# Kernel tuning notes

Hardware: AMD Instinct MI355X
Metric: run time of the kernel (lower is better)

Reference implementation:

```python
import jax, jax.numpy as jnp
import numpy as np


def setup_inputs() -> dict:
    key = jax.random.key(0)
    k1, k2 = jax.random.split(key)
    B, Lq, Ls, D = 16, 2048, 2048, 512
    query = jax.random.normal(k1, (B, Lq, D), dtype=jnp.float32)
    support = jax.random.normal(k2, (B, Ls, D), dtype=jnp.float32)
    return {"query": query, "support": support}


def reference(query, support):
    # attn: [B, Lq, Ls] = softmax(query @ support^T, axis=-1)
    logits = jnp.einsum("bqd,bsd->bqs", query, support)
    attn = jax.nn.softmax(logits, axis=-1)
    # attended support: [B, Lq, D]
    attended = jnp.einsum("bqs,bsd->bqd", attn, support)
    # score: [B, Lq] = sum over D of query * attended
    score = jnp.sum(query * attended, axis=-1)
    return score
```

## Files before the change

kernel.cpp:

```cpp
#include <hip/hip_runtime.h>
#include <hip/hip_bf16.h>

#define B_  16
#define LQ  2048
#define LS  2048
#define DD  512
#define BQ  128
#define BS  256
#define BK  64
#define NSB (LS / BS)
#define NKC (DD / BK)
#define NSPLIT 2

typedef short bf16x8 __attribute__((ext_vector_type(8)));
typedef float f32x4  __attribute__((ext_vector_type(4)));

__device__ __forceinline__ void load_lds16(const void* g, void* l) {
  __builtin_amdgcn_global_load_lds((const __attribute__((address_space(1))) void*)g,
                                   (__attribute__((address_space(3))) void*)l,
                                   16, 0, 0);
}

__device__ __forceinline__ unsigned short f2bf(float f) {
  union { float f; unsigned int u; } v; v.f = f;
  unsigned int r = v.u + 0x7fffu + ((v.u >> 16) & 1u);
  return (unsigned short)(r >> 16);
}

__global__ __launch_bounds__(256) void cvt_kernel(const float* __restrict__ Q,
                                                  const float* __restrict__ S,
                                                  unsigned short* __restrict__ Qw,
                                                  unsigned short* __restrict__ Sw,
                                                  int nblk) {
  int blk = blockIdx.x;
  const float* src; unsigned short* dst;
  if (blk < nblk) { src = Q; dst = Qw; } else { src = S; dst = Sw; blk -= nblk; }
  int i = blk * 256 + threadIdx.x;
  float4 f = ((const float4*)src)[i];
  ushort4 u;
  u.x = f2bf(f.x); u.y = f2bf(f.y); u.z = f2bf(f.z); u.w = f2bf(f.w);
  ((ushort4*)dst)[i] = u;
}

__global__ __launch_bounds__(1024, 4) void attn_kernel(const unsigned short* __restrict__ Qw,
                                                       const unsigned short* __restrict__ Sw,
                                                       float* __restrict__ out,
                                                       float* __restrict__ pm,
                                                       float* __restrict__ pse,
                                                       float* __restrict__ psel,
                                                       int nsplit) {
  __shared__ __align__(16) unsigned short sQ[2][BQ * BK];
  __shared__ __align__(16) unsigned short sS[2][BS * BK];

  const int qb   = blockIdx.x;
  const int b    = blockIdx.y;
  const int spl  = blockIdx.z;
  const int tid  = threadIdx.x;
  const int w    = tid >> 6;
  const int lane = tid & 63;
  const int h    = w & 3;
  const int g    = w >> 2;
  const int col  = lane & 15;
  const int quad = lane >> 4;
  const int c7   = col & 7;

  const int q0 = qb * BQ;
  const unsigned short* Qb = Qw + (size_t)b * LQ * DD;
  const unsigned short* Sb = Sw + (size_t)b * LS * DD;

  float mst[2] = { -INFINITY, -INFINITY };
  float se[2]  = { 0.f, 0.f };
  float sel[2] = { 0.f, 0.f };

  f32x4 acc[4][2];

  const int rr = lane >> 3;
  const int cc = ((lane & 7) ^ rr) * 8;

  const int sbp = NSB / nsplit;
  const int sbs = spl * sbp;
  const int T   = sbp * NKC;

  auto issue = [&](int t, int buf) {
    const int sb = sbs + (t >> 3);
    const int kc = t & 7;
    const int s0 = sb * BS;
    const int kb = kc * BK + cc;
    load_lds16(Qb + (size_t)(q0 + w * 8 + rr) * DD + kb,        &sQ[buf][(w * 8) * BK]);
    load_lds16(Sb + (size_t)(s0 + w * 8 + rr) * DD + kb,        &sS[buf][(w * 8) * BK]);
    load_lds16(Sb + (size_t)(s0 + 128 + w * 8 + rr) * DD + kb,  &sS[buf][(128 + w * 8) * BK]);
  };

  issue(0, 0);

  for (int t = 0; t < T; ++t) {
    const int buf = t & 1;
    __syncthreads();
    if (t + 1 < T) issue(t + 1, buf ^ 1);

    if ((t & 7) == 0) {
#pragma unroll
      for (int st = 0; st < 4; ++st)
#pragma unroll
        for (int qt = 0; qt < 2; ++qt)
          acc[st][qt] = (f32x4){0.f, 0.f, 0.f, 0.f};
    }

#pragma unroll
    for (int kk = 0; kk < 2; ++kk) {
      const int koff = ((kk * 4 + quad) ^ c7) * 8;
      bf16x8 aq[2], asv[4];
#pragma unroll
      for (int qt = 0; qt < 2; ++qt)
        aq[qt] = *(const bf16x8*)&sQ[buf][(g * 32 + qt * 16 + col) * BK + koff];
#pragma unroll
      for (int st = 0; st < 4; ++st)
        asv[st] = *(const bf16x8*)&sS[buf][(h * 64 + st * 16 + col) * BK + koff];
#pragma unroll
      for (int st = 0; st < 4; ++st)
#pragma unroll
        for (int qt = 0; qt < 2; ++qt)
          acc[st][qt] = __builtin_amdgcn_mfma_f32_16x16x32_bf16(asv[st], aq[qt], acc[st][qt], 0, 0, 0);
    }

    if ((t & 7) == 7) {
#pragma unroll
      for (int qt = 0; qt < 2; ++qt) {
        float lmax = mst[qt];
#pragma unroll
        for (int st = 0; st < 4; ++st)
#pragma unroll
          for (int r = 0; r < 4; ++r)
            lmax = fmaxf(lmax, acc[st][qt][r]);
        lmax = fmaxf(lmax, __shfl_xor(lmax, 16, 64));
        lmax = fmaxf(lmax, __shfl_xor(lmax, 32, 64));
        float alpha = __expf(mst[qt] - lmax);
        float pe = 0.f, pel = 0.f;
#pragma unroll
        for (int st = 0; st < 4; ++st)
#pragma unroll
          for (int r = 0; r < 4; ++r) {
            float l = acc[st][qt][r];
            float e = __expf(l - lmax);
            pe += e;
            pel = fmaf(e, l, pel);
          }
        pe  += __shfl_xor(pe, 16, 64);  pe  += __shfl_xor(pe, 32, 64);
        pel += __shfl_xor(pel, 16, 64); pel += __shfl_xor(pel, 32, 64);
        se[qt]  = fmaf(se[qt],  alpha, pe);
        sel[qt] = fmaf(sel[qt], alpha, pel);
        mst[qt] = lmax;
      }
    }
  }

  __syncthreads();
  float* red = (float*)&sQ[0][0];
  if (quad == 0) {
#pragma unroll
    for (int qt = 0; qt < 2; ++qt) {
      int idx = ((g * 4 + h) * 2 + qt) * 16 + col;
      red[idx]        = mst[qt];
      red[512 + idx]  = se[qt];
      red[1024 + idx] = sel[qt];
    }
  }
  __syncthreads();
  if (h == 0 && quad == 0) {
#pragma unroll
    for (int qt = 0; qt < 2; ++qt) {
      float M = -INFINITY;
#pragma unroll
      for (int hh = 0; hh < 4; ++hh)
        M = fmaxf(M, red[((g * 4 + hh) * 2 + qt) * 16 + col]);
      float SE = 0.f, SEL = 0.f;
#pragma unroll
      for (int hh = 0; hh < 4; ++hh) {
        int idx = ((g * 4 + hh) * 2 + qt) * 16 + col;
        float a = __expf(red[idx] - M);
        SE  = fmaf(red[512 + idx],  a, SE);
        SEL = fmaf(red[1024 + idx], a, SEL);
      }
      size_t qi = (size_t)b * LQ + q0 + g * 32 + qt * 16 + col;
      if (nsplit == 1) {
        out[qi] = SEL / SE;
      } else {
        pm[qi * NSPLIT + spl]   = M;
        pse[qi * NSPLIT + spl]  = SE;
        psel[qi * NSPLIT + spl] = SEL;
      }
    }
  }
}

__global__ __launch_bounds__(256) void combine_kernel(const float* __restrict__ pm,
                                                      const float* __restrict__ pse,
                                                      const float* __restrict__ psel,
                                                      float* __restrict__ out) {
  int i = blockIdx.x * blockDim.x + threadIdx.x;
  if (i >= B_ * LQ) return;
  float M = -INFINITY;
#pragma unroll
  for (int s = 0; s < NSPLIT; ++s) M = fmaxf(M, pm[i * NSPLIT + s]);
  float SE = 0.f, SEL = 0.f;
#pragma unroll
  for (int s = 0; s < NSPLIT; ++s) {
    float a = __expf(pm[i * NSPLIT + s] - M);
    SE  = fmaf(pse[i * NSPLIT + s],  a, SE);
    SEL = fmaf(psel[i * NSPLIT + s], a, SEL);
  }
  out[i] = SEL / SE;
}

__global__ __launch_bounds__(256) void fallback_kernel(const float* __restrict__ Q,
                                                       const float* __restrict__ S,
                                                       float* __restrict__ out) {
  __shared__ float qv[DD];
  __shared__ float red[256];
  const int b = blockIdx.y, qi = blockIdx.x, tid = threadIdx.x;
  const float* qrow = Q + ((size_t)b * LQ + qi) * DD;
  for (int d = tid; d < DD; d += 256) qv[d] = qrow[d];
  __syncthreads();
  const float* Sb = S + (size_t)b * LS * DD;
  float m = -INFINITY, se = 0.f, sel = 0.f;
  for (int s = tid; s < LS; s += 256) {
    const float* srow = Sb + (size_t)s * DD;
    float dot = 0.f;
    for (int d = 0; d < DD; ++d) dot = fmaf(qv[d], srow[d], dot);
    float mn = fmaxf(m, dot);
    float a = __expf(m - mn);
    float e = __expf(dot - mn);
    se  = se * a + e;
    sel = sel * a + e * dot;
    m = mn;
  }
  red[tid] = m; __syncthreads();
  for (int o = 128; o > 0; o >>= 1) { if (tid < o) red[tid] = fmaxf(red[tid], red[tid + o]); __syncthreads(); }
  float M = red[0]; __syncthreads();
  float a = __expf(m - M); se *= a; sel *= a;
  red[tid] = se; __syncthreads();
  for (int o = 128; o > 0; o >>= 1) { if (tid < o) red[tid] += red[tid + o]; __syncthreads(); }
  float SE = red[0]; __syncthreads();
  red[tid] = sel; __syncthreads();
  for (int o = 128; o > 0; o >>= 1) { if (tid < o) red[tid] += red[tid + o]; __syncthreads(); }
  float SEL = red[0];
  if (tid == 0) out[(size_t)b * LQ + qi] = SEL / SE;
}

extern "C" void kernel_launch(void* const* d_in, const int* in_sizes, int n_in,
                              void* d_out, int out_size, void* d_ws, size_t ws_size,
                              hipStream_t stream) {
  const float* Q = (const float*)d_in[0];
  const float* S = (const float*)d_in[1];
  float* out = (float*)d_out;
  const size_t nelem = (size_t)B_ * LQ * DD;
  const size_t need_base  = 2 * nelem * sizeof(unsigned short);
  const size_t part_elems = (size_t)B_ * LQ * NSPLIT;
  const size_t need_split = need_base + 3 * part_elems * sizeof(float);

  if (ws_size >= need_base) {
    unsigned short* Qw = (unsigned short*)d_ws;
    unsigned short* Sw = Qw + nelem;
    int nblk = (int)(nelem / 4 / 256);
    cvt_kernel<<<2 * nblk, 256, 0, stream>>>(Q, S, Qw, Sw, nblk);
    if (ws_size >= need_split) {
      float* pm   = (float*)(Sw + nelem);
      float* pse  = pm + part_elems;
      float* psel = pse + part_elems;
      attn_kernel<<<dim3(LQ / BQ, B_, NSPLIT), 1024, 0, stream>>>(Qw, Sw, out, pm, pse, psel, NSPLIT);
      combine_kernel<<<(B_ * LQ + 255) / 256, 256, 0, stream>>>(pm, pse, psel, out);
    } else {
      attn_kernel<<<dim3(LQ / BQ, B_, 1), 1024, 0, stream>>>(Qw, Sw, out, nullptr, nullptr, nullptr, 1);
    }
  } else {
    fallback_kernel<<<dim3(LQ, B_), 256, 0, stream>>>(Q, S, out);
  }
}
```

Measured before the change: 239.7 us.

## Double query tile to 256 rows and specialize warps for Q/S loading

Raises the query tile from 128 to 256 rows, so each wave computes a 4x4 grid of MFMA tiles instead of 4x2. Each support tile loaded into LDS is therefore reused across twice as many queries, which cuts global and LDS traffic per FLOP. Load issue is split so that half the waves stage Q and half stage S. The grid is flattened with batch and split index innermost for locality, and the single-split fallback path is dropped. The cost is double the LDS footprint (128KB), more accumulator registers, and half as many blocks, which may leave the GPU under-filled.

```diff
diff --git a/kernel.cpp b/kernel.cpp
--- a/kernel.cpp
+++ b/kernel.cpp
@@ -5,7 +5,7 @@
 #define LQ  2048
 #define LS  2048
 #define DD  512
-#define BQ  128
+#define BQ  256
 #define BS  256
 #define BK  64
 #define NSB (LS / BS)
@@ -44,17 +44,17 @@
 
 __global__ __launch_bounds__(1024, 4) void attn_kernel(const unsigned short* __restrict__ Qw,
                                                        const unsigned short* __restrict__ Sw,
-                                                       float* __restrict__ out,
                                                        float* __restrict__ pm,
                                                        float* __restrict__ pse,
-                                                       float* __restrict__ psel,
-                                                       int nsplit) {
+                                                       float* __restrict__ psel) {
   __shared__ __align__(16) unsigned short sQ[2][BQ * BK];
   __shared__ __align__(16) unsigned short sS[2][BS * BK];
 
-  const int qb   = blockIdx.x;
-  const int b    = blockIdx.y;
-  const int spl  = blockIdx.z;
+  const int id   = blockIdx.x;
+  const int qb   = id >> 5;
+  const int bs   = id & 31;
+  const int b    = bs >> 1;
+  const int spl  = bs & 1;
   const int tid  = threadIdx.x;
   const int w    = tid >> 6;
   const int lane = tid & 63;
@@ -68,27 +68,33 @@
   const unsigned short* Qb = Qw + (size_t)b * LQ * DD;
   const unsigned short* Sb = Sw + (size_t)b * LS * DD;
 
-  float mst[2] = { -INFINITY, -INFINITY };
-  float se[2]  = { 0.f, 0.f };
-  float sel[2] = { 0.f, 0.f };
-
-  f32x4 acc[4][2];
+  float mst[4] = { -INFINITY, -INFINITY, -INFINITY, -INFINITY };
+  float se[4]  = { 0.f, 0.f, 0.f, 0.f };
+  float sel[4] = { 0.f, 0.f, 0.f, 0.f };
+
+  f32x4 acc[4][4];
 
   const int rr = lane >> 3;
   const int cc = ((lane & 7) ^ rr) * 8;
 
-  const int sbp = NSB / nsplit;
+  const int sbp = NSB / NSPLIT;
   const int sbs = spl * sbp;
   const int T   = sbp * NKC;
 
   auto issue = [&](int t, int buf) {
-    const int sb = sbs + (t >> 3);
-    const int kc = t & 7;
-    const int s0 = sb * BS;
-    const int kb = kc * BK + cc;
-    load_lds16(Qb + (size_t)(q0 + w * 8 + rr) * DD + kb,        &sQ[buf][(w * 8) * BK]);
-    load_lds16(Sb + (size_t)(s0 + w * 8 + rr) * DD + kb,        &sS[buf][(w * 8) * BK]);
-    load_lds16(Sb + (size_t)(s0 + 128 + w * 8 + rr) * DD + kb,  &sS[buf][(128 + w * 8) * BK]);
+    const int kb = (t & 7) * BK + cc;
+    if (w < 8) {
+      const int r0 = w * 32;
+#pragma unroll
+      for (int i = 0; i < 4; ++i)
+        load_lds16(Qb + (size_t)(q0 + r0 + i * 8 + rr) * DD + kb, &sQ[buf][(r0 + i * 8) * BK]);
+    } else {
+      const int s0 = (sbs + (t >> 3)) * BS + (w - 8) * 32;
+      const int l0 = (w - 8) * 32;
+#pragma unroll
+      for (int i = 0; i < 4; ++i)
+        load_lds16(Sb + (size_t)(s0 + i * 8 + rr) * DD + kb, &sS[buf][(l0 + i * 8) * BK]);
+    }
   };
 
   issue(0, 0);
@@ -102,30 +108,30 @@
 #pragma unroll
       for (int st = 0; st < 4; ++st)
 #pragma unroll
-        for (int qt = 0; qt < 2; ++qt)
+        for (int qt = 0; qt < 4; ++qt)
           acc[st][qt] = (f32x4){0.f, 0.f, 0.f, 0.f};
     }
 
 #pragma unroll
     for (int kk = 0; kk < 2; ++kk) {
       const int koff = ((kk * 4 + quad) ^ c7) * 8;
-      bf16x8 aq[2], asv[4];
-#pragma unroll
-      for (int qt = 0; qt < 2; ++qt)
-        aq[qt] = *(const bf16x8*)&sQ[buf][(g * 32 + qt * 16 + col) * BK + koff];
+      bf16x8 aq[4], asv[4];
+#pragma unroll
+      for (int qt = 0; qt < 4; ++qt)
+        aq[qt] = *(const bf16x8*)&sQ[buf][(g * 64 + qt * 16 + col) * BK + koff];
 #pragma unroll
       for (int st = 0; st < 4; ++st)
         asv[st] = *(const bf16x8*)&sS[buf][(h * 64 + st * 16 + col) * BK + koff];
 #pragma unroll
       for (int st = 0; st < 4; ++st)
 #pragma unroll
-        for (int qt = 0; qt < 2; ++qt)
+        for (int qt = 0; qt < 4; ++qt)
           acc[st][qt] = __builtin_amdgcn_mfma_f32_16x16x32_bf16(asv[st], aq[qt], acc[st][qt], 0, 0, 0);
     }
 
     if ((t & 7) == 7) {
 #pragma unroll
-      for (int qt = 0; qt < 2; ++qt) {
+      for (int qt = 0; qt < 4; ++qt) {
         float lmax = mst[qt];
 #pragma unroll
         for (int st = 0; st < 4; ++st)
@@ -158,37 +164,33 @@
   float* red = (float*)&sQ[0][0];
   if (quad == 0) {
 #pragma unroll
-    for (int qt = 0; qt < 2; ++qt) {
-      int idx = ((g * 4 + h) * 2 + qt) * 16 + col;
+    for (int qt = 0; qt < 4; ++qt) {
+      int idx = ((g * 4 + h) * 4 + qt) * 16 + col;
       red[idx]        = mst[qt];
-      red[512 + idx]  = se[qt];
-      red[1024 + idx] = sel[qt];
+      red[1024 + idx] = se[qt];
+      red[2048 + idx] = sel[qt];
     }
   }
   __syncthreads();
   if (h == 0 && quad == 0) {
 #pragma unroll
-    for (int qt = 0; qt < 2; ++qt) {
+    for (int qt = 0; qt < 4; ++qt) {
       float M = -INFINITY;
 #pragma unroll
       for (int hh = 0; hh < 4; ++hh)
-        M = fmaxf(M, red[((g * 4 + hh) * 2 + qt) * 16 + col]);
+        M = fmaxf(M, red[((g * 4 + hh) * 4 + qt) * 16 + col]);
       float SE = 0.f, SEL = 0.f;
 #pragma unroll
       for (int hh = 0; hh < 4; ++hh) {
-        int idx = ((g * 4 + hh) * 2 + qt) * 16 + col;
+        int idx = ((g * 4 + hh) * 4 + qt) * 16 + col;
         float a = __expf(red[idx] - M);
-        SE  = fmaf(red[512 + idx],  a, SE);
-        SEL = fmaf(red[1024 + idx], a, SEL);
+        SE  = fmaf(red[1024 + idx], a, SE);
+        SEL = fmaf(red[2048 + idx], a, SEL);
       }
-      size_t qi = (size_t)b * LQ + q0 + g * 32 + qt * 16 + col;
-      if (nsplit == 1) {
-        out[qi] = SEL / SE;
-      } else {
-        pm[qi * NSPLIT + spl]   = M;
-        pse[qi * NSPLIT + spl]  = SE;
-        psel[qi * NSPLIT + spl] = SEL;
-      }
+      size_t qi = (size_t)b * LQ + q0 + g * 64 + qt * 16 + col;
+      pm[qi * NSPLIT + spl]   = M;
+      pse[qi * NSPLIT + spl]  = SE;
+      psel[qi * NSPLIT + spl] = SEL;
     }
   }
 }
@@ -254,24 +256,20 @@
   const float* S = (const float*)d_in[1];
   float* out = (float*)d_out;
   const size_t nelem = (size_t)B_ * LQ * DD;
-  const size_t need_base  = 2 * nelem * sizeof(unsigned short);
   const size_t part_elems = (size_t)B_ * LQ * NSPLIT;
-  const size_t need_split = need_base + 3 * part_elems * sizeof(float);
-
-  if (ws_size >= need_base) {
+  const size_t need = 2 * nelem * sizeof(unsigned short)
+                    + 3 * part_elems * sizeof(float);
+
+  if (ws_size >= need) {
     unsigned short* Qw = (unsigned short*)d_ws;
     unsigned short* Sw = Qw + nelem;
+    float* pm   = (float*)(Sw + nelem);
+    float* pse  = pm + part_elems;
+    float* psel = pse + part_elems;
     int nblk = (int)(nelem / 4 / 256);
     cvt_kernel<<<2 * nblk, 256, 0, stream>>>(Q, S, Qw, Sw, nblk);
-    if (ws_size >= need_split) {
-      float* pm   = (float*)(Sw + nelem);
-      float* pse  = pm + part_elems;
-      float* psel = pse + part_elems;
-      attn_kernel<<<dim3(LQ / BQ, B_, NSPLIT), 1024, 0, stream>>>(Qw, Sw, out, pm, pse, psel, NSPLIT);
-      combine_kernel<<<(B_ * LQ + 255) / 256, 256, 0, stream>>>(pm, pse, psel, out);
-    } else {
-      attn_kernel<<<dim3(LQ / BQ, B_, 1), 1024, 0, stream>>>(Qw, Sw, out, nullptr, nullptr, nullptr, 1);
-    }
+    attn_kernel<<<(LQ / BQ) * B_ * NSPLIT, 1024, 0, stream>>>(Qw, Sw, pm, pse, psel);
+    combine_kernel<<<(B_ * LQ + 255) / 256, 256, 0, stream>>>(pm, pse, psel, out);
   } else {
     fallback_kernel<<<dim3(LQ, B_), 256, 0, stream>>>(Q, S, out);
   }
```

Measured after the change: 238.0 us. No clear change (-0.7%).
